# Performance work log

Hardware: AMD Instinct MI355X
Metric: run time of the kernel (lower is better)

The kernel has to match this reference:

```python
import jax, jax.numpy as jnp
import numpy as np

NVOC, NIN, NHID = 10000, 1024, 256
T, B = 128, 64


def setup_inputs() -> dict:
    key = jax.random.key(0)
    ks = jax.random.split(key, 12)

    def nrm(k, shape, s=0.05):
        return (jax.random.normal(k, shape) * s).astype(jnp.float32)

    z = lambda *s: jnp.zeros(s, jnp.float32)
    att_scale = 2.0 / np.sqrt(NHID)
    return {
        "tokens": jax.random.randint(ks[0], (T, B), 0, NVOC),
        "E": nrm(ks[1], (NVOC, NIN), 0.1),            # embedding table
        "Wih1": nrm(ks[2], (3 * NHID, NIN)),          # GRU1 input weights (r,z,n)
        "Whh1": nrm(ks[3], (3 * NHID, NHID)),
        "bih1": z(3 * NHID), "bhh1": z(3 * NHID),
        "Wih2": nrm(ks[4], (3 * NHID, NHID + NIN)),   # GRU2 input weights
        "Whh2": nrm(ks[5], (3 * NHID, NHID)),
        "bih2": z(3 * NHID), "bhh2": z(3 * NHID),
        "Wh": nrm(ks[6], (NHID, NHID)), "bh": z(NHID),   # attention linear_hid
        "Wi": nrm(ks[7], (NHID, NHID)), "bi": z(NHID),   # attention linear_input
        "w_att": nrm(ks[8], (NHID,), att_scale),          # attention score vector
        "Wd": nrm(ks[9], (NVOC, NHID), 0.1), "bd": z(NVOC),  # decoder
    }


def _gru_cell(h, xg, Whh, bhh):
    # xg: [B, 3H] precomputed input gates; PyTorch gate order (r, z, n)
    H = h.shape[-1]
    hg = h @ Whh.T + bhh
    r = jax.nn.sigmoid(xg[:, :H] + hg[:, :H])
    zt = jax.nn.sigmoid(xg[:, H:2 * H] + hg[:, H:2 * H])
    n = jnp.tanh(xg[:, 2 * H:] + r * hg[:, 2 * H:])
    return (1.0 - zt) * n + zt * h


def reference(tokens, E, Wih1, Whh1, bih1, bhh1, Wih2, Whh2, bih2, bhh2,
              Wh, bh, Wi, bi, w_att, Wd, bd):
    Tn, Bn = tokens.shape
    H = Whh1.shape[-1]
    emb = E[tokens]                                  # [T,B,NIN] (dropout = eval identity)

    # ---- rnn_1 over full sequence ----
    xg1 = emb @ Wih1.T + bih1                        # [T,B,3H]
    def step1(h, xg_t):
        h_new = _gru_cell(h, xg_t, Whh1, bhh1)
        return h_new, h_new
    h1, out1 = jax.lax.scan(step1, jnp.zeros((Bn, H), emb.dtype), xg1)
    # h1: final hidden [B,H]; out1: [T,B,H]

    # linear_hid on rnn_1 outputs (prefix slices of this equal per-step recompute)
    proj = out1 @ Wh.T + bh                          # [T,B,H]
    tidx = jnp.arange(Tn)
    neg_inf = jnp.asarray(-jnp.inf, proj.dtype)

    # ---- decode loop with growing-window additive attention ----
    def step2(h2, inputs):
        t, emb_t = inputs
        q = h2 @ Wi.T + bi                           # [B,H]
        scores = jnp.sum(jnp.tanh(proj + q[None]) * w_att, axis=2)   # [T,B]
        scores = jnp.where(tidx[:, None] <= t, scores, neg_inf)
        energy = jax.nn.softmax(scores, axis=0)      # [T,B], prefix softmax
        # hidden[:i+1] with nlayers=1 is always the [1,B,H] final rnn_1 hidden
        state = jnp.sum(energy[:, :, None] * h1[None], axis=0)       # [B,H]
        x = jnp.concatenate([state, emb_t], axis=1)  # [B, H+NIN]
        xg = x @ Wih2.T + bih2
        h2_new = _gru_cell(h2, xg, Whh2, bhh2)
        return h2_new, h2_new                        # pred == new hidden (1-layer GRU)

    _, preds = jax.lax.scan(step2, jnp.zeros((Bn, H), emb.dtype), (tidx, emb))
    # decoder (dropout = identity in eval)
    logits = preds @ Wd.T + bd                       # [T,B,NVOC]
    return logits, h1[None]                          # hidden returned as [1,B,H]
```

## Files before the change

kernel.cpp:

```cpp
#include <hip/hip_runtime.h>
#include <cstdint>
#include <cstddef>

#define DI __device__ __forceinline__

typedef short bf16x8 __attribute__((ext_vector_type(8)));
typedef float f32x4  __attribute__((ext_vector_type(4)));
typedef _Float16 half2v __attribute__((ext_vector_type(2)));

typedef const uint32_t __attribute__((address_space(1)))* gptr_t;
typedef uint32_t       __attribute__((address_space(3)))* lptr_t;

DI void load_lds16(const void* g, void* l_wave_uniform) {
#if __has_builtin(__builtin_amdgcn_global_load_lds)
  __builtin_amdgcn_global_load_lds((gptr_t)g, (lptr_t)l_wave_uniform, 16, 0, 0);
#else
  int lane = threadIdx.x & 63;
  *(uint4*)((char*)l_wave_uniform + lane * 16) = *(const uint4*)g;
#endif
}

DI ushort f2bf(float f) {
  uint32_t u = __builtin_bit_cast(uint32_t, f);
  u += 0x7fffu + ((u >> 16) & 1u);
  return (ushort)(u >> 16);
}

DI half2v h2cast(uint32_t u) { return __builtin_bit_cast(half2v, u); }

#if __has_builtin(__builtin_amdgcn_fdot2)
#define FDOT2(a, b, c) __builtin_amdgcn_fdot2((a), (b), (c), false)
#else
DI float fdot2_fb(half2v a, half2v b, float c) {
  return c + (float)a.x * (float)b.x + (float)a.y * (float)b.y;
}
#define FDOT2(a, b, c) fdot2_fb((a), (b), (c))
#endif


__global__ void cvt_w1cat(const float* __restrict__ W1, const float* __restrict__ W2,
                          ushort* __restrict__ dst) {
  int idx = blockIdx.x * 256 + threadIdx.x;
  int e = idx * 4;
  int row = e >> 10;
  int col = e & 1023;
  const float* src = (row < 768) ? (W1 + (size_t)row * 1024 + col)
                                 : (W2 + (size_t)(row - 768) * 1280 + 256 + col);
  float4 f = *(const float4*)src;
  ushort4 o; o.x = f2bf(f.x); o.y = f2bf(f.y); o.z = f2bf(f.z); o.w = f2bf(f.w);
  *(ushort4*)(dst + e) = o;
}

__global__ void cvt_wd(const float* __restrict__ Wd, ushort* __restrict__ dst) {
  int idx = blockIdx.x * 256 + threadIdx.x;
  int e = idx * 4;
  int row = e >> 8;
  int col = e & 255;
  ushort4 o;
  if (row < 10000) {
    float4 f = *(const float4*)(Wd + (size_t)row * 256 + col);
    o.x = f2bf(f.x); o.y = f2bf(f.y); o.z = f2bf(f.z); o.w = f2bf(f.w);
  } else {
    o.x = 0; o.y = 0; o.z = 0; o.w = 0;
  }
  *(ushort4*)(dst + e) = o;
}

__global__ void cvt_whh(const float* __restrict__ W, uint32_t* __restrict__ dst) {
  int idx = blockIdx.x * 256 + threadIdx.x;
  int row = idx >> 7;
  int p = idx & 127;
  float2 f = *(const float2*)(W + (size_t)row * 256 + p * 2);
  half2v h; h.x = (_Float16)f.x; h.y = (_Float16)f.y;
  dst[idx] = __builtin_bit_cast(uint32_t, h);
}

__global__ void gather_emb(const int* __restrict__ tok, const float* __restrict__ E,
                           ushort* __restrict__ emb) {
  int row = blockIdx.x;
  int t = threadIdx.x;
  int v = tok[row];
  float4 f = *((const float4*)(E + (size_t)v * 1024) + t);
  ushort4 o; o.x = f2bf(f.x); o.y = f2bf(f.y); o.z = f2bf(f.z); o.w = f2bf(f.w);
  *((ushort4*)(emb + (size_t)row * 1024) + t) = o;
}

template <bool BIAS, bool GUARD>
__global__ __launch_bounds__(256) void gemm_bt(
    const ushort* __restrict__ A, const ushort* __restrict__ B,
    float* __restrict__ C, const float* __restrict__ bias, int M, int K, int Nout) {
  __shared__ __align__(16) ushort As[128 * 64];
  __shared__ __align__(16) ushort Bs[128 * 64];
  const int t = threadIdx.x;
  const int wave = t >> 6, lane = t & 63;
  const int m0 = blockIdx.x * 128, n0 = blockIdx.y * 128;
  const int RM = (wave >> 1) * 64, RN = (wave & 1) * 64;
  const int lm = lane & 15, kg = lane >> 4;

  f32x4 acc[4][4] = {};

  for (int k0 = 0; k0 < K; k0 += 64) {
#pragma unroll
    for (int i = 0; i < 4; ++i) {
      int off = i * 4096 + t * 16;
      int row = off >> 7;
      int physc = (off >> 4) & 7;
      int gc = physc ^ (row & 7);
      int ub = i * 4096 + wave * 1024;
      const ushort* ga = A + (size_t)(m0 + row) * K + k0 + gc * 8;
      load_lds16(ga, (char*)As + ub);
      const ushort* gb = B + (size_t)(n0 + row) * K + k0 + gc * 8;
      load_lds16(gb, (char*)Bs + ub);
    }
    __syncthreads();
#pragma unroll
    for (int kk = 0; kk < 64; kk += 32) {
      const int lc = (kk >> 3) + kg;
      bf16x8 af[4], bfr[4];
#pragma unroll
      for (int i = 0; i < 4; ++i) {
        int ra = RM + i * 16 + lm;
        int rb = RN + i * 16 + lm;
        af[i]  = *(const bf16x8*)(As + ra * 64 + ((lc ^ (ra & 7)) << 3));
        bfr[i] = *(const bf16x8*)(Bs + rb * 64 + ((lc ^ (rb & 7)) << 3));
      }
#pragma unroll
      for (int i = 0; i < 4; ++i)
#pragma unroll
        for (int j = 0; j < 4; ++j)
          acc[i][j] = __builtin_amdgcn_mfma_f32_16x16x32_bf16(af[i], bfr[j], acc[i][j], 0, 0, 0);
    }
    __syncthreads();
  }

  const int rg = lane >> 4;
#pragma unroll
  for (int i = 0; i < 4; ++i) {
    int grow = m0 + RM + i * 16 + rg * 4;
#pragma unroll
    for (int j = 0; j < 4; ++j) {
      int gcol = n0 + RN + j * 16 + lm;
      if (GUARD && gcol >= Nout) continue;
      float bv = BIAS ? bias[gcol] : 0.f;
#pragma unroll
      for (int r = 0; r < 4; ++r)
        C[(size_t)(grow + r) * Nout + gcol] = acc[i][j][r] + bv;
    }
  }
}

__global__ __launch_bounds__(768, 3) void gru_scan(
    const uint32_t* __restrict__ Wpk,
    const float* __restrict__ xg_all,
    int xg_off,
    const float* __restrict__ bih, const float* __restrict__ bhh,
    const float* __restrict__ Wih2,
    const float* __restrict__ h1in,
    float* __restrict__ hfin_ws,
    float* __restrict__ hfin_out,
    ushort* __restrict__ preds)
{
  const int b = blockIdx.x;
  const int j = threadIdx.x;
  __shared__ __align__(16) uint32_t hpk[128];
  __shared__ float rz[512];

  float xbase = bih[j];
  const float bhhj = bhh[j];
  if (Wih2) {
    const float4* wr = (const float4*)(Wih2 + (size_t)j * 1280);
    const float4* hb = (const float4*)(h1in + b * 256);
    float s = 0.f;
#pragma unroll 2
    for (int k = 0; k < 64; ++k) {
      float4 a = wr[k], c = hb[k];
      s += a.x * c.x + a.y * c.y + a.z * c.z + a.w * c.w;
    }
    xbase += s;
  }

  uint4 w[32];
  {
    const uint4* wp = (const uint4*)(Wpk + (size_t)j * 128);
#pragma unroll
    for (int i = 0; i < 32; ++i) w[i] = wp[i];
  }

  if (j < 128) hpk[j] = 0u;
  float hprev = 0.f;
  __syncthreads();

  const float* xgp = xg_all + (size_t)b * 1536 + xg_off + j;
  float xcur = xgp[0];

  for (int t = 0; t < 128; ++t) {
    int tn = (t + 1 < 128) ? t + 1 : 127;
    float xnext = xgp[(size_t)tn * 98304];

    float a0 = 0.f, a1 = 0.f, a2 = 0.f, a3 = 0.f;
#pragma unroll
    for (int i = 0; i < 32; ++i) {
      uint4 hv = ((const uint4*)hpk)[i];
      a0 = FDOT2(h2cast(w[i].x), h2cast(hv.x), a0);
      a1 = FDOT2(h2cast(w[i].y), h2cast(hv.y), a1);
      a2 = FDOT2(h2cast(w[i].z), h2cast(hv.z), a2);
      a3 = FDOT2(h2cast(w[i].w), h2cast(hv.w), a3);
    }
    float hg = (a0 + a1) + (a2 + a3) + bhhj;
    float xgv = xcur + xbase;

    if (j < 512) rz[j] = 1.f / (1.f + __expf(-(xgv + hg)));
    __syncthreads();
    if (j >= 512) {
      int j2 = j - 512;
      float r = rz[j2], z = rz[256 + j2];
      float x2 = xgv + r * hg;
      x2 = fminf(fmaxf(x2, -15.f), 15.f);
      float e = __expf(-2.f * x2);
      float n = (1.f - e) / (1.f + e);
      float hnew = (1.f - z) * n + z * hprev;
      hprev = hnew;
      if (preds) preds[(size_t)(t * 64 + b) * 256 + j2] = f2bf(hnew);
      float hup = __shfl_down(hnew, 1);
      if (!(j2 & 1)) {
        half2v hh; hh.x = (_Float16)hnew; hh.y = (_Float16)hup;
        hpk[j2 >> 1] = __builtin_bit_cast(uint32_t, hh);
      }
    }
    xcur = xnext;
    __syncthreads();
  }

  if (j >= 512) {
    int j2 = j - 512;
    if (hfin_ws)  hfin_ws[b * 256 + j2] = hprev;
    if (hfin_out) hfin_out[b * 256 + j2] = hprev;
  }
}

extern "C" void kernel_launch(void* const* d_in, const int* in_sizes, int n_in,
                              void* d_out, int out_size, void* d_ws, size_t ws_size,
                              hipStream_t stream) {
  const int*   tokens = (const int*)d_in[0];
  const float* E      = (const float*)d_in[1];
  const float* Wih1   = (const float*)d_in[2];
  const float* Whh1   = (const float*)d_in[3];
  const float* bih1   = (const float*)d_in[4];
  const float* bhh1   = (const float*)d_in[5];
  const float* Wih2   = (const float*)d_in[6];
  const float* Whh2   = (const float*)d_in[7];
  const float* bih2   = (const float*)d_in[8];
  const float* bhh2   = (const float*)d_in[9];
  const float* Wd     = (const float*)d_in[15];
  const float* bd     = (const float*)d_in[16];
  float* out = (float*)d_out;

  char* ws = (char*)d_ws;
  ushort*   emb   = (ushort*)  (ws + 0);
  ushort*   w1cat = (ushort*)  (ws + 16777216);
  float*    xg    = (float*)   (ws + 19922944);
  ushort*   wdb   = (ushort*)  (ws + 70254592);
  uint32_t* whh1p = (uint32_t*)(ws + 75431936);
  uint32_t* whh2p = (uint32_t*)(ws + 75825152);
  float*    h1    = (float*)   (ws + 76218368);
  ushort*   preds = (ushort*)  (ws + 76283904);

  cvt_w1cat<<<1536, 256, 0, stream>>>(Wih1, Wih2, w1cat);
  cvt_wd<<<2528, 256, 0, stream>>>(Wd, wdb);
  cvt_whh<<<384, 256, 0, stream>>>(Whh1, whh1p);
  cvt_whh<<<384, 256, 0, stream>>>(Whh2, whh2p);
  gather_emb<<<8192, 256, 0, stream>>>(tokens, E, emb);

  dim3 g1(64, 12);
  gemm_bt<false, false><<<g1, 256, 0, stream>>>(emb, w1cat, xg, nullptr, 8192, 1024, 1536);

  gru_scan<<<64, 768, 0, stream>>>(whh1p, xg, 0, bih1, bhh1,
                                   nullptr, nullptr, h1, out + 81920000, nullptr);
  gru_scan<<<64, 768, 0, stream>>>(whh2p, xg, 768, bih2, bhh2,
                                   Wih2, h1, nullptr, nullptr, preds);

  dim3 g2(64, 79);
  gemm_bt<true, true><<<g2, 256, 0, stream>>>(preds, wdb, out, bd, 8192, 256, 10000);
}
```

Baseline: 882.4 us.

## Restructure GRU scan so thread pairs compute all three gates with one barrier

The recurrent GRU kernel moves from 768 threads (one gate row each, with an LDS exchange of r/z and two barriers per step) to 512 threads. Each adjacent thread pair splits the K dimension for the r, z and n rows of one hidden unit and combines partial sums and gate values with lane shuffles. The hidden state is double-buffered in LDS so each timestep needs only one barrier. The two Whh conversion launches are merged into one. The cost is 192 weight registers per thread and extra shuffles, which may lower occupancy or cause spills.

```diff
diff --git a/kernel.cpp b/kernel.cpp
--- a/kernel.cpp
+++ b/kernel.cpp
@@ -66,10 +66,14 @@
   *(ushort4*)(dst + e) = o;
 }
 
-__global__ void cvt_whh(const float* __restrict__ W, uint32_t* __restrict__ dst) {
+__global__ void cvt_whh(const float* __restrict__ W1, const float* __restrict__ W2,
+                        uint32_t* __restrict__ dst) {
   int idx = blockIdx.x * 256 + threadIdx.x;
-  int row = idx >> 7;
-  int p = idx & 127;
+  const float* W = W1;
+  int i = idx;
+  if (i >= 98304) { W = W2; i -= 98304; }
+  int row = i >> 7;
+  int p = i & 127;
   float2 f = *(const float2*)(W + (size_t)row * 256 + p * 2);
   half2v h; h.x = (_Float16)f.x; h.y = (_Float16)f.y;
   dst[idx] = __builtin_bit_cast(uint32_t, h);
@@ -149,7 +153,7 @@
   }
 }
 
-__global__ __launch_bounds__(768, 3) void gru_scan(
+__global__ __launch_bounds__(512, 2) void gru_scan(
     const uint32_t* __restrict__ Wpk,
     const float* __restrict__ xg_all,
     int xg_off,
@@ -161,80 +165,104 @@
     ushort* __restrict__ preds)
 {
   const int b = blockIdx.x;
-  const int j = threadIdx.x;
-  __shared__ __align__(16) uint32_t hpk[128];
-  __shared__ float rz[512];
-
-  float xbase = bih[j];
-  const float bhhj = bhh[j];
+  const int t0 = threadIdx.x;
+  const int j = t0 >> 1;
+  const int half = t0 & 1;
+  __shared__ __align__(16) uint32_t hpk[2][128];
+
+  const int rowA = half ? 512 + j : j;
+  const int rowB = half ? 512 + j : 256 + j;
+
+  float xb0 = bih[rowA], xb1 = bih[rowB];
+  const float bh0 = bhh[rowA], bh1 = bhh[rowB];
+
   if (Wih2) {
-    const float4* wr = (const float4*)(Wih2 + (size_t)j * 1280);
     const float4* hb = (const float4*)(h1in + b * 256);
-    float s = 0.f;
+    const float4* wa = (const float4*)(Wih2 + (size_t)rowA * 1280);
+    const float4* wb = (const float4*)(Wih2 + (size_t)rowB * 1280);
+    float sa = 0.f, sb = 0.f;
 #pragma unroll 2
     for (int k = 0; k < 64; ++k) {
-      float4 a = wr[k], c = hb[k];
-      s += a.x * c.x + a.y * c.y + a.z * c.z + a.w * c.w;
-    }
-    xbase += s;
-  }
-
-  uint4 w[32];
+      float4 h4 = hb[k], a4 = wa[k], b4 = wb[k];
+      sa += a4.x * h4.x + a4.y * h4.y + a4.z * h4.z + a4.w * h4.w;
+      sb += b4.x * h4.x + b4.y * h4.y + b4.z * h4.z + b4.w * h4.w;
+    }
+    xb0 += sa; xb1 += sb;
+  }
+
+  uint4 wr[16], wz[16], wn[16];
   {
-    const uint4* wp = (const uint4*)(Wpk + (size_t)j * 128);
-#pragma unroll
-    for (int i = 0; i < 32; ++i) w[i] = wp[i];
-  }
-
-  if (j < 128) hpk[j] = 0u;
+    const uint4* wp = (const uint4*)Wpk;
+    const uint4* pr_ = wp + (size_t)j * 32 + half * 16;
+    const uint4* pz_ = wp + (size_t)(256 + j) * 32 + half * 16;
+    const uint4* pn_ = wp + (size_t)(512 + j) * 32 + half * 16;
+#pragma unroll
+    for (int i = 0; i < 16; ++i) { wr[i] = pr_[i]; wz[i] = pz_[i]; wn[i] = pn_[i]; }
+  }
+
+  if (t0 < 128) hpk[0][t0] = 0u;
   float hprev = 0.f;
   __syncthreads();
 
-  const float* xgp = xg_all + (size_t)b * 1536 + xg_off + j;
-  float xcur = xgp[0];
+  const float* xp0 = xg_all + (size_t)b * 1536 + xg_off + rowA;
+  const float* xp1 = xg_all + (size_t)b * 1536 + xg_off + rowB;
+  float xc0 = xp0[0], xc1 = xp1[0];
+  ushort* pout = preds ? (preds + (size_t)b * 256 + j) : nullptr;
 
   for (int t = 0; t < 128; ++t) {
-    int tn = (t + 1 < 128) ? t + 1 : 127;
-    float xnext = xgp[(size_t)tn * 98304];
-
-    float a0 = 0.f, a1 = 0.f, a2 = 0.f, a3 = 0.f;
-#pragma unroll
-    for (int i = 0; i < 32; ++i) {
-      uint4 hv = ((const uint4*)hpk)[i];
-      a0 = FDOT2(h2cast(w[i].x), h2cast(hv.x), a0);
-      a1 = FDOT2(h2cast(w[i].y), h2cast(hv.y), a1);
-      a2 = FDOT2(h2cast(w[i].z), h2cast(hv.z), a2);
-      a3 = FDOT2(h2cast(w[i].w), h2cast(hv.w), a3);
-    }
-    float hg = (a0 + a1) + (a2 + a3) + bhhj;
-    float xgv = xcur + xbase;
-
-    if (j < 512) rz[j] = 1.f / (1.f + __expf(-(xgv + hg)));
+    const int tn = (t + 1 < 128) ? t + 1 : 127;
+    float xn0 = xp0[(size_t)tn * 98304];
+    float xn1 = xp1[(size_t)tn * 98304];
+
+    float pr0 = 0.f, pr1 = 0.f, pz0 = 0.f, pz1 = 0.f, pn0 = 0.f, pn1 = 0.f;
+    const uint4* hb = (const uint4*)(hpk[t & 1]) + half * 16;
+#pragma unroll
+    for (int i = 0; i < 16; ++i) {
+      uint4 hv = hb[i];
+      pr0 = FDOT2(h2cast(wr[i].x), h2cast(hv.x), pr0);
+      pz0 = FDOT2(h2cast(wz[i].x), h2cast(hv.x), pz0);
+      pn0 = FDOT2(h2cast(wn[i].x), h2cast(hv.x), pn0);
+      pr1 = FDOT2(h2cast(wr[i].y), h2cast(hv.y), pr1);
+      pz1 = FDOT2(h2cast(wz[i].y), h2cast(hv.y), pz1);
+      pn1 = FDOT2(h2cast(wn[i].y), h2cast(hv.y), pn1);
+      pr0 = FDOT2(h2cast(wr[i].z), h2cast(hv.z), pr0);
+      pz0 = FDOT2(h2cast(wz[i].z), h2cast(hv.z), pz0);
+      pn0 = FDOT2(h2cast(wn[i].z), h2cast(hv.z), pn0);
+      pr1 = FDOT2(h2cast(wr[i].w), h2cast(hv.w), pr1);
+      pz1 = FDOT2(h2cast(wz[i].w), h2cast(hv.w), pz1);
+      pn1 = FDOT2(h2cast(wn[i].w), h2cast(hv.w), pn1);
+    }
+    float hr = pr0 + pr1, hz = pz0 + pz1, hn = pn0 + pn1;
+    hr += __shfl_xor(hr, 1);
+    hz += __shfl_xor(hz, 1);
+    hn += __shfl_xor(hn, 1);
+
+    float s0 = 1.f / (1.f + __expf(-(xc0 + xb0 + hr + bh0)));
+    float s1 = 1.f / (1.f + __expf(-(xc1 + xb1 + hz + bh1)));
+    float rv = __shfl_xor(s0, 1);
+    float zv = __shfl_xor(s1, 1);
+
+    float x2 = xc0 + xb0 + rv * (hn + bh0);
+    x2 = fminf(fmaxf(x2, -15.f), 15.f);
+    float e = __expf(-2.f * x2);
+    float nn = (1.f - e) / (1.f + e);
+    float hnew = (1.f - zv) * nn + zv * hprev;
+    float hup = __shfl_xor(hnew, 2);
+    if (half) {
+      hprev = hnew;
+      if (pout) pout[(size_t)t * 16384] = f2bf(hnew);
+      if ((t0 & 2) == 0) {
+        half2v hh; hh.x = (_Float16)hnew; hh.y = (_Float16)hup;
+        hpk[(t + 1) & 1][t0 >> 2] = __builtin_bit_cast(uint32_t, hh);
+      }
+    }
+    xc0 = xn0; xc1 = xn1;
     __syncthreads();
-    if (j >= 512) {
-      int j2 = j - 512;
-      float r = rz[j2], z = rz[256 + j2];
-      float x2 = xgv + r * hg;
-      x2 = fminf(fmaxf(x2, -15.f), 15.f);
-      float e = __expf(-2.f * x2);
-      float n = (1.f - e) / (1.f + e);
-      float hnew = (1.f - z) * n + z * hprev;
-      hprev = hnew;
-      if (preds) preds[(size_t)(t * 64 + b) * 256 + j2] = f2bf(hnew);
-      float hup = __shfl_down(hnew, 1);
-      if (!(j2 & 1)) {
-        half2v hh; hh.x = (_Float16)hnew; hh.y = (_Float16)hup;
-        hpk[j2 >> 1] = __builtin_bit_cast(uint32_t, hh);
-      }
-    }
-    xcur = xnext;
-    __syncthreads();
-  }
-
-  if (j >= 512) {
-    int j2 = j - 512;
-    if (hfin_ws)  hfin_ws[b * 256 + j2] = hprev;
-    if (hfin_out) hfin_out[b * 256 + j2] = hprev;
+  }
+
+  if (half) {
+    if (hfin_ws)  hfin_ws[b * 256 + j] = hprev;
+    if (hfin_out) hfin_out[b * 256 + j] = hprev;
   }
 }
 
@@ -267,16 +295,15 @@
 
   cvt_w1cat<<<1536, 256, 0, stream>>>(Wih1, Wih2, w1cat);
   cvt_wd<<<2528, 256, 0, stream>>>(Wd, wdb);
-  cvt_whh<<<384, 256, 0, stream>>>(Whh1, whh1p);
-  cvt_whh<<<384, 256, 0, stream>>>(Whh2, whh2p);
+  cvt_whh<<<768, 256, 0, stream>>>(Whh1, Whh2, whh1p);
   gather_emb<<<8192, 256, 0, stream>>>(tokens, E, emb);
 
   dim3 g1(64, 12);
   gemm_bt<false, false><<<g1, 256, 0, stream>>>(emb, w1cat, xg, nullptr, 8192, 1024, 1536);
 
-  gru_scan<<<64, 768, 0, stream>>>(whh1p, xg, 0, bih1, bhh1,
+  gru_scan<<<64, 512, 0, stream>>>(whh1p, xg, 0, bih1, bhh1,
                                    nullptr, nullptr, h1, out + 81920000, nullptr);
-  gru_scan<<<64, 768, 0, stream>>>(whh2p, xg, 768, bih2, bhh2,
+  gru_scan<<<64, 512, 0, stream>>>(whh2p, xg, 768, bih2, bhh2,
                                    Wih2, h1, nullptr, nullptr, preds);
 
   dim3 g2(64, 79);
```

Result: no change. 872.4 us (-1.1%).
